# Performance work log

Measured on AMD Instinct MI355X. Metric: run time of the kernel, lower is better.

Reference implementation:

```python
import jax, jax.numpy as jnp
import numpy as np

B, S, D, H = 4, 2048, 512, 8
DH = D // H  # 64


def setup_inputs() -> dict:
    key = jax.random.key(0)
    ks = jax.random.split(key, 7)
    scale = 1.0 / np.sqrt(D)
    return {
        "in_query": jax.random.normal(ks[0], (B, S, D), dtype=jnp.float32),
        "in_key": jax.random.normal(ks[1], (B, S, D), dtype=jnp.float32),
        "in_value": jax.random.normal(ks[2], (B, S, D), dtype=jnp.float32),
        "W_q": jax.random.normal(ks[3], (D, D), dtype=jnp.float32) * scale,
        "W_k": jax.random.normal(ks[4], (D, D), dtype=jnp.float32) * scale,
        "W_v": jax.random.normal(ks[5], (D, D), dtype=jnp.float32) * scale,
        "W_out": jax.random.normal(ks[6], (D, D), dtype=jnp.float32) * scale,
    }


def _split_heads(x):
    # [B, S, D] -> [B, H, S, DH]
    return x.reshape(B, S, H, DH).transpose(0, 2, 1, 3)


def reference(in_query, in_key, in_value, W_q, W_k, W_v, W_out):
    q = _split_heads(in_query @ W_q)   # [B,H,S,DH]
    k = _split_heads(in_key @ W_k)
    v = _split_heads(in_value @ W_v)
    scores = jnp.einsum("bhqd,bhkd->bhqk", q, k) / jnp.sqrt(jnp.float32(DH))
    attn = jax.nn.softmax(scores, axis=-1)  # dropout p=0 -> identity
    out = jnp.einsum("bhqk,bhkd->bhqd", attn, v)  # [B,H,S,DH]
    out = out.transpose(0, 2, 1, 3).reshape(B, S, D)
    return out @ W_out
```

## Files before the change

kernel.cpp:

```cpp
#include <hip/hip_runtime.h>
#include <hip/hip_bf16.h>
#include <cstdint>
#include <cstddef>


typedef __bf16 bf16;
typedef __attribute__((ext_vector_type(8))) __bf16 bf16x8;
typedef __attribute__((ext_vector_type(4))) __bf16 bf16x4;
typedef __attribute__((ext_vector_type(4))) float floatx4;

#define MFMA16(a, b, c) __builtin_amdgcn_mfma_f32_16x16x32_bf16(a, b, c, 0, 0, 0)

#define GLD16(gp, lp)                                              \
  __builtin_amdgcn_global_load_lds(                                \
      (const __attribute__((address_space(1))) unsigned int*)(gp), \
      (__attribute__((address_space(3))) unsigned int*)(lp), 16, 0, 0)

__device__ __forceinline__ void split2(float x, bf16& hi, bf16& lo) {
  hi = (bf16)x;
  lo = (bf16)(x - (float)hi);
}

__global__ __launch_bounds__(256) void k_split_w(
    const float* __restrict__ Wq, const float* __restrict__ Wk,
    const float* __restrict__ Wv, const float* __restrict__ Wo,
    bf16* __restrict__ wt_hi, bf16* __restrict__ wt_lo) {
  __shared__ float tile[64][65];
  const int w = blockIdx.z;
  const float* W = (w == 0) ? Wq : (w == 1) ? Wk : (w == 2) ? Wv : Wo;
  const int kb = blockIdx.y * 64, nb = blockIdx.x * 64;
  const int tid = threadIdx.x;
  const int col = tid & 63, rbase = tid >> 6;
#pragma unroll
  for (int i = 0; i < 16; i++) {
    int row = rbase + i * 4;
    tile[row][col] = W[(size_t)(kb + row) * 512 + nb + col];
  }
  __syncthreads();
#pragma unroll
  for (int i = 0; i < 16; i++) {
    int nrow = rbase + i * 4;
    float v = tile[col][nrow];
    bf16 hi, lo;
    split2(v, hi, lo);
    size_t o = (size_t)w * 262144 + (size_t)(nb + nrow) * 512 + (kb + col);
    wt_hi[o] = hi;
    wt_lo[o] = lo;
  }
}

__global__ __launch_bounds__(256) void k_proj_qkv(
    const float* __restrict__ Xq, const float* __restrict__ Xk,
    const float* __restrict__ Xv,
    const bf16* __restrict__ wt_hi, const bf16* __restrict__ wt_lo,
    bf16* __restrict__ Q_hi, bf16* __restrict__ Q_lo,
    bf16* __restrict__ K_hi, bf16* __restrict__ K_lo,
    bf16* __restrict__ Vt) {
  const int P = blockIdx.x;
  const int c_all = P >> 5, within = P & 31;
  const int n_idx = within >> 3, i8 = within & 7;
  const int which = c_all >> 3;
  const int g = ((c_all & 7) << 3) | i8;
  const int m0 = g * 128, n0 = n_idx * 128;

  const float* X = (which == 0) ? Xq : (which == 1) ? Xk : Xv;
  const uint8_t* Bhb = (const uint8_t*)(wt_hi + (size_t)which * 262144);
  const uint8_t* Blb = (const uint8_t*)(wt_lo + (size_t)which * 262144);
  const uint8_t* Xb = (const uint8_t*)X;
  const int tid = threadIdx.x, wave = tid >> 6, lane = tid & 63;
  const int l15 = lane & 15, l4 = lane >> 4;
  const int Am0 = (wave & 1) * 64, Bn0 = (wave >> 1) * 64;

  __shared__ float sA[128 * 32];
  __shared__ bf16 sBh[128 * 32], sBl[128 * 32];

  int aoff[4], adst[4];
#pragma unroll
  for (int p = 0; p < 4; p++) {
    int slot = p * 256 + tid;
    int row = slot >> 3, phys = slot & 7, lg = phys ^ (row & 7);
    aoff[p] = (m0 + row) * 2048 + lg * 16;
    adst[p] = slot * 16;
  }
  int boff[2], bdst[2];
#pragma unroll
  for (int p = 0; p < 2; p++) {
    int slot = p * 256 + tid;
    int row = slot >> 2, phys = slot & 3, lg = phys ^ (row & 3);
    boff[p] = (n0 + row) * 1024 + lg * 16;
    bdst[p] = slot * 16;
  }

  floatx4 acc[4][4];
#pragma unroll
  for (int i = 0; i < 4; i++)
#pragma unroll
    for (int j = 0; j < 4; j++) acc[i][j] = {0.f, 0.f, 0.f, 0.f};

  for (int kb = 0; kb < 512; kb += 32) {
    __syncthreads();
#pragma unroll
    for (int p = 0; p < 4; p++) GLD16(Xb + aoff[p] + kb * 4, (char*)sA + adst[p]);
#pragma unroll
    for (int p = 0; p < 2; p++) {
      GLD16(Bhb + boff[p] + kb * 2, (char*)sBh + bdst[p]);
      GLD16(Blb + boff[p] + kb * 2, (char*)sBl + bdst[p]);
    }
    __syncthreads();

    bf16x8 ah[4], al[4];
#pragma unroll
    for (int mt = 0; mt < 4; mt++) {
      int row = Am0 + mt * 16 + l15, r7 = row & 7;
      const float* f0 = (const float*)((const char*)sA + row * 128 + (((2 * l4) ^ r7) * 16));
      const float* f1 = (const float*)((const char*)sA + row * 128 + (((2 * l4 + 1) ^ r7) * 16));
#pragma unroll
      for (int j = 0; j < 4; j++) {
        bf16 h, l;
        split2(f0[j], h, l);
        ah[mt][j] = h; al[mt][j] = l;
        split2(f1[j], h, l);
        ah[mt][4 + j] = h; al[mt][4 + j] = l;
      }
    }
#pragma unroll
    for (int nt = 0; nt < 4; nt++) {
      int row = Bn0 + nt * 16 + l15, r3 = row & 3;
      bf16x8 bh = *(const bf16x8*)((const char*)sBh + row * 64 + ((l4 ^ r3) * 16));
      bf16x8 bl = *(const bf16x8*)((const char*)sBl + row * 64 + ((l4 ^ r3) * 16));
#pragma unroll
      for (int mt = 0; mt < 4; mt++) {
        acc[mt][nt] = MFMA16(ah[mt], bh, acc[mt][nt]);
        acc[mt][nt] = MFMA16(ah[mt], bl, acc[mt][nt]);
        acc[mt][nt] = MFMA16(al[mt], bh, acc[mt][nt]);
      }
    }
  }

  const float scale = (which == 0) ? 0.125f : (which == 1) ? 1.44269504f : 1.0f;
#pragma unroll
  for (int mt = 0; mt < 4; mt++) {
#pragma unroll
    for (int nt = 0; nt < 4; nt++) {
      int m_base = m0 + Am0 + mt * 16 + l4 * 4;
      int n = n0 + Bn0 + nt * 16 + l15;
      int h = (n >> 6) & 7, d = n & 63;
      if (which == 2) {
        int kbase = m_base & 2047, b = m_base >> 11;
        int a32 = kbase & ~31, v = (kbase >> 2) & 7;
        int sbase = a32 + 8 * (v & 3) + 4 * (v >> 2);
        bf16x4 pv;
#pragma unroll
        for (int r = 0; r < 4; r++) pv[r] = (bf16)acc[mt][nt][r];
        *(bf16x4*)&Vt[((size_t)(b * 8 + h) * 64 + d) * 2048 + sbase] = pv;
      } else {
#pragma unroll
        for (int r = 0; r < 4; r++) {
          int m = m_base + r;
          int b = m >> 11, s = m & 2047;
          float v = acc[mt][nt][r] * scale;
          bf16 hi, lo;
          split2(v, hi, lo);
          size_t o = ((size_t)(b * 8 + h) * 2048 + s) * 64 + d;
          if (which == 0) { Q_hi[o] = hi; Q_lo[o] = lo; }
          else           { K_hi[o] = hi; K_lo[o] = lo; }
        }
      }
    }
  }
}

__global__ __launch_bounds__(256, 2) void k_flash(
    const bf16* __restrict__ Q_hi, const bf16* __restrict__ Q_lo,
    const bf16* __restrict__ K_hi, const bf16* __restrict__ K_lo,
    const bf16* __restrict__ Vt,
    bf16* __restrict__ O_hi, bf16* __restrict__ O_lo) {
  const int P = blockIdx.x;
  const int hi4 = P >> 8, rem = P & 255;
  const int qt = rem >> 3;
  const int bh = hi4 * 8 + (rem & 7);
  const int b = bh >> 3, h = bh & 7;
  const int tid = threadIdx.x, wave = tid >> 6, lane = tid & 63;
  const int l15 = lane & 15, l4 = lane >> 4;
  const int q0 = qt * 64;

  __shared__ bf16 sKh[128 * 64];
  __shared__ bf16 sKl[128 * 64];
  __shared__ bf16 sV[64 * 128];

  bf16x8 qh[4][2], ql[4][2];
#pragma unroll
  for (int nt = 0; nt < 4; nt++) {
    const bf16* ph = Q_hi + ((size_t)bh * 2048 + q0 + nt * 16 + l15) * 64 + l4 * 8;
    const bf16* pl = Q_lo + ((size_t)bh * 2048 + q0 + nt * 16 + l15) * 64 + l4 * 8;
    qh[nt][0] = *(const bf16x8*)ph;
    qh[nt][1] = *(const bf16x8*)(ph + 32);
    ql[nt][0] = *(const bf16x8*)pl;
    ql[nt][1] = *(const bf16x8*)(pl + 32);
  }

  const uint8_t* Khb = (const uint8_t*)K_hi + (size_t)bh * 2048 * 128;
  const uint8_t* Klb = (const uint8_t*)K_lo + (size_t)bh * 2048 * 128;
  const uint8_t* Vb = (const uint8_t*)Vt + (size_t)bh * 64 * 4096;
  int koff[4], voff[4], dst[4];
#pragma unroll
  for (int p = 0; p < 4; p++) {
    int slot = p * 256 + tid;
    {
      int row = slot >> 3, phys = slot & 7, lg = phys ^ (row & 7);
      koff[p] = row * 128 + lg * 16;
    }
    {
      int row = slot >> 4, phys = slot & 15, lg = phys ^ (row & 15);
      voff[p] = row * 4096 + lg * 16;
    }
    dst[p] = slot * 16;
  }

  float lp[4] = {0.f, 0.f, 0.f, 0.f};
  floatx4 oacc[4][4];
#pragma unroll
  for (int i = 0; i < 4; i++)
#pragma unroll
    for (int j = 0; j < 4; j++) oacc[i][j] = {0.f, 0.f, 0.f, 0.f};

  for (int j0 = 0; j0 < 2048; j0 += 128) {
    __syncthreads();
#pragma unroll
    for (int p = 0; p < 4; p++) {
      GLD16(Khb + (size_t)j0 * 128 + koff[p], (char*)sKh + dst[p]);
      GLD16(Klb + (size_t)j0 * 128 + koff[p], (char*)sKl + dst[p]);
      GLD16(Vb + (size_t)j0 * 2 + voff[p], (char*)sV + dst[p]);
    }
    __syncthreads();

    floatx4 sc[2][4];
#pragma unroll
    for (int kt = 0; kt < 2; kt++)
#pragma unroll
      for (int nt = 0; nt < 4; nt++) sc[kt][nt] = {0.f, 0.f, 0.f, 0.f};
#pragma unroll
    for (int kt = 0; kt < 2; kt++) {
      int row = wave * 32 + kt * 16 + l15;
      int r7 = row & 7;
#pragma unroll
      for (int ks = 0; ks < 2; ks++) {
        int off = row * 128 + (((ks * 4 + l4) ^ r7) * 16);
        bf16x8 kh = *(const bf16x8*)((const char*)sKh + off);
        bf16x8 kl = *(const bf16x8*)((const char*)sKl + off);
#pragma unroll
        for (int nt = 0; nt < 4; nt++) {
          sc[kt][nt] = MFMA16(kh, qh[nt][ks], sc[kt][nt]);
          sc[kt][nt] = MFMA16(kl, qh[nt][ks], sc[kt][nt]);
          sc[kt][nt] = MFMA16(kh, ql[nt][ks], sc[kt][nt]);
        }
      }
    }

    bf16x8 pf[4];
#pragma unroll
    for (int nt = 0; nt < 4; nt++) {
#pragma unroll
      for (int r = 0; r < 4; r++) {
        float p0 = __builtin_amdgcn_exp2f(sc[0][nt][r]);
        float p1 = __builtin_amdgcn_exp2f(sc[1][nt][r]);
        lp[nt] += p0 + p1;
        pf[nt][r] = (bf16)p0;
        pf[nt][4 + r] = (bf16)p1;
      }
    }

#pragma unroll
    for (int nt = 0; nt < 4; nt++) {
      int row = nt * 16 + l15;
      int off = row * 256 + (((wave * 4 + l4) ^ l15) * 16);
      bf16x8 bv = *(const bf16x8*)((const char*)sV + off);
#pragma unroll
      for (int mq = 0; mq < 4; mq++)
        oacc[mq][nt] = MFMA16(pf[mq], bv, oacc[mq][nt]);
    }
  }

#pragma unroll
  for (int nt = 0; nt < 4; nt++) {
    lp[nt] += __shfl_xor(lp[nt], 16, 64);
    lp[nt] += __shfl_xor(lp[nt], 32, 64);
  }
  float* lbuf = (float*)sV;
  floatx4* red0 = (floatx4*)sKh;
  floatx4* red1 = (floatx4*)sKl;
  __syncthreads();
  if (l4 == 0) {
#pragma unroll
    for (int nt = 0; nt < 4; nt++) lbuf[wave * 64 + nt * 16 + l15] = lp[nt];
  }
  if (wave == 2) {
#pragma unroll
    for (int i = 0; i < 16; i++) red0[i * 64 + lane] = oacc[i >> 2][i & 3];
  }
  if (wave == 3) {
#pragma unroll
    for (int i = 0; i < 16; i++) red1[i * 64 + lane] = oacc[i >> 2][i & 3];
  }
  __syncthreads();
  if (wave == 0) {
#pragma unroll
    for (int i = 0; i < 16; i++) oacc[i >> 2][i & 3] += red0[i * 64 + lane];
  }
  if (wave == 1) {
#pragma unroll
    for (int i = 0; i < 16; i++) oacc[i >> 2][i & 3] += red1[i * 64 + lane];
  }
  __syncthreads();
  if (wave == 1) {
#pragma unroll
    for (int i = 0; i < 16; i++) red0[i * 64 + lane] = oacc[i >> 2][i & 3];
  }
  __syncthreads();
  if (wave == 0) {
#pragma unroll
    for (int i = 0; i < 16; i++) oacc[i >> 2][i & 3] += red0[i * 64 + lane];
    float lt[4];
#pragma unroll
    for (int nt = 0; nt < 4; nt++)
      lt[nt] = lbuf[nt * 16 + l15] + lbuf[64 + nt * 16 + l15] +
               lbuf[128 + nt * 16 + l15] + lbuf[192 + nt * 16 + l15];
    float rl[4][4];
#pragma unroll
    for (int mq = 0; mq < 4; mq++)
#pragma unroll
      for (int r = 0; r < 4; r++)
        rl[mq][r] = 1.0f / __shfl(lt[mq], (lane & 48) | (l4 * 4 + r), 64);
#pragma unroll
    for (int mq = 0; mq < 4; mq++) {
#pragma unroll
      for (int nt = 0; nt < 4; nt++) {
#pragma unroll
        for (int r = 0; r < 4; r++) {
          float v = oacc[mq][nt][r] * rl[mq][r];
          int gs = q0 + mq * 16 + l4 * 4 + r;
          int gd = h * 64 + nt * 16 + l15;
          size_t o = ((size_t)b * 2048 + gs) * 512 + gd;
          bf16 hi, lo;
          split2(v, hi, lo);
          O_hi[o] = hi;
          O_lo[o] = lo;
        }
      }
    }
  }
}

__global__ __launch_bounds__(256) void k_proj_out(
    const bf16* __restrict__ O_hi, const bf16* __restrict__ O_lo,
    const bf16* __restrict__ wt_hi, const bf16* __restrict__ wt_lo,
    float* __restrict__ out) {
  const int P = blockIdx.x;
  const int c = P >> 5, within = P & 31;
  const int n_idx = within >> 3, i8 = within & 7;
  const int g = (c << 3) | i8;
  const int m0 = g * 128, n0 = n_idx * 128;

  const uint8_t* Ahb = (const uint8_t*)O_hi;
  const uint8_t* Alb = (const uint8_t*)O_lo;
  const uint8_t* Bhb = (const uint8_t*)(wt_hi + (size_t)3 * 262144);
  const uint8_t* Blb = (const uint8_t*)(wt_lo + (size_t)3 * 262144);
  const int tid = threadIdx.x, wave = tid >> 6, lane = tid & 63;
  const int l15 = lane & 15, l4 = lane >> 4;
  const int Am0 = (wave & 1) * 64, Bn0 = (wave >> 1) * 64;

  __shared__ bf16 sAh[128 * 32], sAl[128 * 32];
  __shared__ bf16 sBh[128 * 32], sBl[128 * 32];

  int aoff[2], boff[2], dst[2];
#pragma unroll
  for (int p = 0; p < 2; p++) {
    int slot = p * 256 + tid;
    int row = slot >> 2, phys = slot & 3, lg = phys ^ (row & 3);
    aoff[p] = (m0 + row) * 1024 + lg * 16;
    boff[p] = (n0 + row) * 1024 + lg * 16;
    dst[p] = slot * 16;
  }

  floatx4 acc[4][4];
#pragma unroll
  for (int i = 0; i < 4; i++)
#pragma unroll
    for (int j = 0; j < 4; j++) acc[i][j] = {0.f, 0.f, 0.f, 0.f};

  for (int kb = 0; kb < 512; kb += 32) {
    __syncthreads();
#pragma unroll
    for (int p = 0; p < 2; p++) {
      GLD16(Ahb + aoff[p] + kb * 2, (char*)sAh + dst[p]);
      GLD16(Alb + aoff[p] + kb * 2, (char*)sAl + dst[p]);
      GLD16(Bhb + boff[p] + kb * 2, (char*)sBh + dst[p]);
      GLD16(Blb + boff[p] + kb * 2, (char*)sBl + dst[p]);
    }
    __syncthreads();

    bf16x8 ah[4], al[4];
#pragma unroll
    for (int mt = 0; mt < 4; mt++) {
      int row = Am0 + mt * 16 + l15, r3 = row & 3;
      ah[mt] = *(const bf16x8*)((const char*)sAh + row * 64 + ((l4 ^ r3) * 16));
      al[mt] = *(const bf16x8*)((const char*)sAl + row * 64 + ((l4 ^ r3) * 16));
    }
#pragma unroll
    for (int nt = 0; nt < 4; nt++) {
      int row = Bn0 + nt * 16 + l15, r3 = row & 3;
      bf16x8 bh = *(const bf16x8*)((const char*)sBh + row * 64 + ((l4 ^ r3) * 16));
      bf16x8 bl = *(const bf16x8*)((const char*)sBl + row * 64 + ((l4 ^ r3) * 16));
#pragma unroll
      for (int mt = 0; mt < 4; mt++) {
        acc[mt][nt] = MFMA16(ah[mt], bh, acc[mt][nt]);
        acc[mt][nt] = MFMA16(ah[mt], bl, acc[mt][nt]);
        acc[mt][nt] = MFMA16(al[mt], bh, acc[mt][nt]);
      }
    }
  }
#pragma unroll
  for (int mt = 0; mt < 4; mt++) {
#pragma unroll
    for (int nt = 0; nt < 4; nt++) {
#pragma unroll
      for (int r = 0; r < 4; r++) {
        int m = m0 + Am0 + mt * 16 + l4 * 4 + r;
        int n = n0 + Bn0 + nt * 16 + l15;
        out[(size_t)m * 512 + n] = acc[mt][nt][r];
      }
    }
  }
}

extern "C" void kernel_launch(void* const* d_in, const int* in_sizes, int n_in,
                              void* d_out, int out_size, void* d_ws, size_t ws_size,
                              hipStream_t stream) {
  (void)in_sizes; (void)n_in; (void)out_size; (void)ws_size;
  const float* Xq = (const float*)d_in[0];
  const float* Xk = (const float*)d_in[1];
  const float* Xv = (const float*)d_in[2];
  const float* Wq = (const float*)d_in[3];
  const float* Wk = (const float*)d_in[4];
  const float* Wv = (const float*)d_in[5];
  const float* Wo = (const float*)d_in[6];
  float* out = (float*)d_out;

  char* ws = (char*)d_ws;
  size_t off = 0;
  auto alloc = [&](size_t n) {
    void* p = ws + off;
    off += (n + 255) & ~(size_t)255;
    return p;
  };
  const size_t NW = 4 * 262144;
  const size_t NE = 4194304;
  bf16* wt_hi = (bf16*)alloc(NW * 2);
  bf16* wt_lo = (bf16*)alloc(NW * 2);
  bf16* Qh = (bf16*)alloc(NE * 2);
  bf16* Ql = (bf16*)alloc(NE * 2);
  bf16* Kh = (bf16*)alloc(NE * 2);
  bf16* Kl = (bf16*)alloc(NE * 2);
  bf16* Vt = (bf16*)alloc(NE * 2);
  bf16* Oh = (bf16*)alloc(NE * 2);
  bf16* Ol = (bf16*)alloc(NE * 2);

  k_split_w<<<dim3(8, 8, 4), dim3(256), 0, stream>>>(Wq, Wk, Wv, Wo, wt_hi, wt_lo);
  k_proj_qkv<<<dim3(768), dim3(256), 0, stream>>>(Xq, Xk, Xv, wt_hi, wt_lo,
                                                  Qh, Ql, Kh, Kl, Vt);
  k_flash<<<dim3(1024), dim3(256), 0, stream>>>(Qh, Ql, Kh, Kl, Vt, Oh, Ol);
  k_proj_out<<<dim3(256), dim3(256), 0, stream>>>(Oh, Ol, wt_hi, wt_lo, out);
}
```

Measured before the change: 233.1 us.

## Load K and V fragments directly from global memory instead of LDS staging

```diff
diff --git a/kernel.cpp b/kernel.cpp
--- a/kernel.cpp
+++ b/kernel.cpp
@@ -184,9 +184,8 @@
   const int l15 = lane & 15, l4 = lane >> 4;
   const int q0 = qt * 64;
 
-  __shared__ bf16 sKh[128 * 64];
-  __shared__ bf16 sKl[128 * 64];
-  __shared__ bf16 sV[64 * 128];
+  __shared__ floatx4 red[3][1024];
+  __shared__ float lbuf[256];
 
   bf16x8 qh[4][2], ql[4][2];
 #pragma unroll
@@ -199,23 +198,9 @@
     ql[nt][1] = *(const bf16x8*)(pl + 32);
   }
 
-  const uint8_t* Khb = (const uint8_t*)K_hi + (size_t)bh * 2048 * 128;
-  const uint8_t* Klb = (const uint8_t*)K_lo + (size_t)bh * 2048 * 128;
-  const uint8_t* Vb = (const uint8_t*)Vt + (size_t)bh * 64 * 4096;
-  int koff[4], voff[4], dst[4];
-#pragma unroll
-  for (int p = 0; p < 4; p++) {
-    int slot = p * 256 + tid;
-    {
-      int row = slot >> 3, phys = slot & 7, lg = phys ^ (row & 7);
-      koff[p] = row * 128 + lg * 16;
-    }
-    {
-      int row = slot >> 4, phys = slot & 15, lg = phys ^ (row & 15);
-      voff[p] = row * 4096 + lg * 16;
-    }
-    dst[p] = slot * 16;
-  }
+  const bf16* Kh0 = K_hi + ((size_t)bh * 2048 + wave * 32 + l15) * 64 + l4 * 8;
+  const bf16* Kl0 = K_lo + ((size_t)bh * 2048 + wave * 32 + l15) * 64 + l4 * 8;
+  const bf16* Vv0 = Vt + ((size_t)bh * 64 + l15) * 2048 + (wave * 4 + l4) * 8;
 
   float lp[4] = {0.f, 0.f, 0.f, 0.f};
   floatx4 oacc[4][4];
@@ -225,14 +210,18 @@
     for (int j = 0; j < 4; j++) oacc[i][j] = {0.f, 0.f, 0.f, 0.f};
 
   for (int j0 = 0; j0 < 2048; j0 += 128) {
-    __syncthreads();
-#pragma unroll
-    for (int p = 0; p < 4; p++) {
-      GLD16(Khb + (size_t)j0 * 128 + koff[p], (char*)sKh + dst[p]);
-      GLD16(Klb + (size_t)j0 * 128 + koff[p], (char*)sKl + dst[p]);
-      GLD16(Vb + (size_t)j0 * 2 + voff[p], (char*)sV + dst[p]);
-    }
-    __syncthreads();
+    bf16x8 kh[2][2], kl[2][2];
+#pragma unroll
+    for (int kt = 0; kt < 2; kt++)
+#pragma unroll
+      for (int ks = 0; ks < 2; ks++) {
+        kh[kt][ks] = *(const bf16x8*)(Kh0 + (size_t)(j0 + kt * 16) * 64 + ks * 32);
+        kl[kt][ks] = *(const bf16x8*)(Kl0 + (size_t)(j0 + kt * 16) * 64 + ks * 32);
+      }
+    bf16x8 bv[4];
+#pragma unroll
+    for (int nt = 0; nt < 4; nt++)
+      bv[nt] = *(const bf16x8*)(Vv0 + (size_t)(nt * 16) * 2048 + j0);
 
     floatx4 sc[2][4];
 #pragma unroll
@@ -240,22 +229,15 @@
 #pragma unroll
       for (int nt = 0; nt < 4; nt++) sc[kt][nt] = {0.f, 0.f, 0.f, 0.f};
 #pragma unroll
-    for (int kt = 0; kt < 2; kt++) {
-      int row = wave * 32 + kt * 16 + l15;
-      int r7 = row & 7;
-#pragma unroll
-      for (int ks = 0; ks < 2; ks++) {
-        int off = row * 128 + (((ks * 4 + l4) ^ r7) * 16);
-        bf16x8 kh = *(const bf16x8*)((const char*)sKh + off);
-        bf16x8 kl = *(const bf16x8*)((const char*)sKl + off);
+    for (int kt = 0; kt < 2; kt++)
+#pragma unroll
+      for (int ks = 0; ks < 2; ks++)
 #pragma unroll
         for (int nt = 0; nt < 4; nt++) {
-          sc[kt][nt] = MFMA16(kh, qh[nt][ks], sc[kt][nt]);
-          sc[kt][nt] = MFMA16(kl, qh[nt][ks], sc[kt][nt]);
-          sc[kt][nt] = MFMA16(kh, ql[nt][ks], sc[kt][nt]);
+          sc[kt][nt] = MFMA16(kh[kt][ks], qh[nt][ks], sc[kt][nt]);
+          sc[kt][nt] = MFMA16(kl[kt][ks], qh[nt][ks], sc[kt][nt]);
+          sc[kt][nt] = MFMA16(kh[kt][ks], ql[nt][ks], sc[kt][nt]);
         }
-      }
-    }
 
     bf16x8 pf[4];
 #pragma unroll
@@ -271,14 +253,10 @@
     }
 
 #pragma unroll
-    for (int nt = 0; nt < 4; nt++) {
-      int row = nt * 16 + l15;
-      int off = row * 256 + (((wave * 4 + l4) ^ l15) * 16);
-      bf16x8 bv = *(const bf16x8*)((const char*)sV + off);
+    for (int nt = 0; nt < 4; nt++)
 #pragma unroll
       for (int mq = 0; mq < 4; mq++)
-        oacc[mq][nt] = MFMA16(pf[mq], bv, oacc[mq][nt]);
-    }
+        oacc[mq][nt] = MFMA16(pf[mq], bv[nt], oacc[mq][nt]);
   }
 
 #pragma unroll
@@ -286,40 +264,20 @@
     lp[nt] += __shfl_xor(lp[nt], 16, 64);
     lp[nt] += __shfl_xor(lp[nt], 32, 64);
   }
-  float* lbuf = (float*)sV;
-  floatx4* red0 = (floatx4*)sKh;
-  floatx4* red1 = (floatx4*)sKl;
-  __syncthreads();
   if (l4 == 0) {
 #pragma unroll
     for (int nt = 0; nt < 4; nt++) lbuf[wave * 64 + nt * 16 + l15] = lp[nt];
   }
-  if (wave == 2) {
-#pragma unroll
-    for (int i = 0; i < 16; i++) red0[i * 64 + lane] = oacc[i >> 2][i & 3];
-  }
-  if (wave == 3) {
-#pragma unroll
-    for (int i = 0; i < 16; i++) red1[i * 64 + lane] = oacc[i >> 2][i & 3];
+  if (wave >= 1) {
+#pragma unroll
+    for (int i = 0; i < 16; i++) red[wave - 1][i * 64 + lane] = oacc[i >> 2][i & 3];
   }
   __syncthreads();
   if (wave == 0) {
 #pragma unroll
-    for (int i = 0; i < 16; i++) oacc[i >> 2][i & 3] += red0[i * 64 + lane];
-  }
-  if (wave == 1) {
-#pragma unroll
-    for (int i = 0; i < 16; i++) oacc[i >> 2][i & 3] += red1[i * 64 + lane];
-  }
-  __syncthreads();
-  if (wave == 1) {
-#pragma unroll
-    for (int i = 0; i < 16; i++) red0[i * 64 + lane] = oacc[i >> 2][i & 3];
-  }
-  __syncthreads();
-  if (wave == 0) {
-#pragma unroll
-    for (int i = 0; i < 16; i++) oacc[i >> 2][i & 3] += red0[i * 64 + lane];
+    for (int i = 0; i < 16; i++)
+      oacc[i >> 2][i & 3] += red[0][i * 64 + lane] + red[1][i * 64 + lane] +
+                             red[2][i * 64 + lane];
     float lt[4];
 #pragma unroll
     for (int nt = 0; nt < 4; nt++)
```

After: 257.3 us. 10.4% more time.

## Load K_lo directly to registers, shrink LDS, raise flash occupancy to 4

Applied to the files above, without the earlier changes.

```diff
diff --git a/kernel.cpp b/kernel.cpp
--- a/kernel.cpp
+++ b/kernel.cpp
@@ -170,7 +170,7 @@
   }
 }
 
-__global__ __launch_bounds__(256, 2) void k_flash(
+__global__ __launch_bounds__(256, 4) void k_flash(
     const bf16* __restrict__ Q_hi, const bf16* __restrict__ Q_lo,
     const bf16* __restrict__ K_hi, const bf16* __restrict__ K_lo,
     const bf16* __restrict__ Vt,
@@ -184,9 +184,10 @@
   const int l15 = lane & 15, l4 = lane >> 4;
   const int q0 = qt * 64;
 
-  __shared__ bf16 sKh[128 * 64];
-  __shared__ bf16 sKl[128 * 64];
-  __shared__ bf16 sV[64 * 128];
+  __shared__ char smem[33792];
+  bf16* sKh = (bf16*)smem;
+  bf16* sV = (bf16*)(smem + 16384);
+  float* lbuf = (float*)(smem + 32768);
 
   bf16x8 qh[4][2], ql[4][2];
 #pragma unroll
@@ -200,8 +201,8 @@
   }
 
   const uint8_t* Khb = (const uint8_t*)K_hi + (size_t)bh * 2048 * 128;
-  const uint8_t* Klb = (const uint8_t*)K_lo + (size_t)bh * 2048 * 128;
   const uint8_t* Vb = (const uint8_t*)Vt + (size_t)bh * 64 * 4096;
+  const bf16* Kl0 = K_lo + ((size_t)bh * 2048 + wave * 32 + l15) * 64 + l4 * 8;
   int koff[4], voff[4], dst[4];
 #pragma unroll
   for (int p = 0; p < 4; p++) {
@@ -229,30 +230,35 @@
 #pragma unroll
     for (int p = 0; p < 4; p++) {
       GLD16(Khb + (size_t)j0 * 128 + koff[p], (char*)sKh + dst[p]);
-      GLD16(Klb + (size_t)j0 * 128 + koff[p], (char*)sKl + dst[p]);
       GLD16(Vb + (size_t)j0 * 2 + voff[p], (char*)sV + dst[p]);
     }
+    bf16x8 kl[2][2];
+#pragma unroll
+    for (int kt = 0; kt < 2; kt++)
+#pragma unroll
+      for (int ks = 0; ks < 2; ks++)
+        kl[kt][ks] = *(const bf16x8*)(Kl0 + (size_t)(j0 + kt * 16) * 64 + ks * 32);
     __syncthreads();
 
     floatx4 sc[2][4];
 #pragma unroll
     for (int kt = 0; kt < 2; kt++)
 #pragma unroll
-      for (int nt = 0; nt < 4; nt++) sc[kt][nt] = {0.f, 0.f, 0.f, 0.f};
+      for (int nt = 0; nt < 4; nt++)
+        sc[kt][nt] = {-24.f, -24.f, -24.f, -24.f};
 #pragma unroll
     for (int kt = 0; kt < 2; kt++) {
       int row = wave * 32 + kt * 16 + l15;
       int r7 = row & 7;
 #pragma unroll
       for (int ks = 0; ks < 2; ks++) {
-        int off = row * 128 + (((ks * 4 + l4) ^ r7) * 16);
-        bf16x8 kh = *(const bf16x8*)((const char*)sKh + off);
-        bf16x8 kl = *(const bf16x8*)((const char*)sKl + off);
+        bf16x8 kh = *(const bf16x8*)((const char*)sKh +
+                                     (row * 128 + (((ks * 4 + l4) ^ r7) * 16)));
 #pragma unroll
         for (int nt = 0; nt < 4; nt++) {
           sc[kt][nt] = MFMA16(kh, qh[nt][ks], sc[kt][nt]);
-          sc[kt][nt] = MFMA16(kl, qh[nt][ks], sc[kt][nt]);
           sc[kt][nt] = MFMA16(kh, ql[nt][ks], sc[kt][nt]);
+          sc[kt][nt] = MFMA16(kl[kt][ks], qh[nt][ks], sc[kt][nt]);
         }
       }
     }
@@ -273,8 +279,8 @@
 #pragma unroll
     for (int nt = 0; nt < 4; nt++) {
       int row = nt * 16 + l15;
-      int off = row * 256 + (((wave * 4 + l4) ^ l15) * 16);
-      bf16x8 bv = *(const bf16x8*)((const char*)sV + off);
+      bf16x8 bv = *(const bf16x8*)((const char*)sV +
+                                   (row * 256 + (((wave * 4 + l4) ^ l15) * 16)));
 #pragma unroll
       for (int mq = 0; mq < 4; mq++)
         oacc[mq][nt] = MFMA16(pf[mq], bv, oacc[mq][nt]);
@@ -286,40 +292,33 @@
     lp[nt] += __shfl_xor(lp[nt], 16, 64);
     lp[nt] += __shfl_xor(lp[nt], 32, 64);
   }
-  float* lbuf = (float*)sV;
-  floatx4* red0 = (floatx4*)sKh;
-  floatx4* red1 = (floatx4*)sKl;
   __syncthreads();
   if (l4 == 0) {
 #pragma unroll
     for (int nt = 0; nt < 4; nt++) lbuf[wave * 64 + nt * 16 + l15] = lp[nt];
   }
-  if (wave == 2) {
-#pragma unroll
-    for (int i = 0; i < 16; i++) red0[i * 64 + lane] = oacc[i >> 2][i & 3];
-  }
-  if (wave == 3) {
-#pragma unroll
-    for (int i = 0; i < 16; i++) red1[i * 64 + lane] = oacc[i >> 2][i & 3];
-  }
-  __syncthreads();
+  floatx4* red = (floatx4*)smem;
+#pragma unroll
+  for (int phase = 0; phase < 2; phase++) {
+    if (wave >= 1) {
+#pragma unroll
+      for (int i = 0; i < 8; i++) {
+        int mq = phase * 2 + (i >> 2);
+        red[(wave - 1) * 512 + i * 64 + lane] = oacc[mq][i & 3];
+      }
+    }
+    __syncthreads();
+    if (wave == 0) {
+#pragma unroll
+      for (int i = 0; i < 8; i++) {
+        int mq = phase * 2 + (i >> 2);
+        oacc[mq][i & 3] += red[i * 64 + lane] + red[512 + i * 64 + lane] +
+                           red[1024 + i * 64 + lane];
+      }
+    }
+    __syncthreads();
+  }
   if (wave == 0) {
-#pragma unroll
-    for (int i = 0; i < 16; i++) oacc[i >> 2][i & 3] += red0[i * 64 + lane];
-  }
-  if (wave == 1) {
-#pragma unroll
-    for (int i = 0; i < 16; i++) oacc[i >> 2][i & 3] += red1[i * 64 + lane];
-  }
-  __syncthreads();
-  if (wave == 1) {
-#pragma unroll
-    for (int i = 0; i < 16; i++) red0[i * 64 + lane] = oacc[i >> 2][i & 3];
-  }
-  __syncthreads();
-  if (wave == 0) {
-#pragma unroll
-    for (int i = 0; i < 16; i++) oacc[i >> 2][i & 3] += red0[i * 64 + lane];
     float lt[4];
 #pragma unroll
     for (int nt = 0; nt < 4; nt++)
```

New measurement: 679.6 us. +191.6%, slower.
